# Kernel optimization log

Hardware: AMD Instinct MI355X
Metric: run time of the kernel (lower is better)

## Reference

```python
import jax, jax.numpy as jnp
import numpy as np

B, T, C, H = 2, 2048, 1024, 16
D = C // H  # head dim 64

def setup_inputs() -> dict:
    key = jax.random.key(0)
    k1, k2, k3 = jax.random.split(key, 3)
    x = jax.random.normal(k1, (B, T, C), dtype=jnp.float32)
    W_attn = jax.random.normal(k2, (C, 3 * C), dtype=jnp.float32) * (1.0 / np.sqrt(C))
    b_attn = jnp.zeros((3 * C,), dtype=jnp.float32)
    W_proj = jax.random.normal(k3, (C, C), dtype=jnp.float32) * (1.0 / np.sqrt(C))
    b_proj = jnp.zeros((C,), dtype=jnp.float32)
    return {"x": x, "W_attn": W_attn, "b_attn": b_attn, "W_proj": W_proj, "b_proj": b_proj}

def reference(x, W_attn, b_attn, W_proj, b_proj):
    Bsz, Tlen, Cdim = x.shape
    qkv = x @ W_attn + b_attn  # [B,T,3C]
    q, k, v = jnp.split(qkv, 3, axis=2)
    # [B,T,C] -> [B,H,T,D]
    q = q.reshape(Bsz, Tlen, H, D).transpose(0, 2, 1, 3)
    k = k.reshape(Bsz, Tlen, H, D).transpose(0, 2, 1, 3)
    v = v.reshape(Bsz, Tlen, H, D).transpose(0, 2, 1, 3)
    att = jnp.einsum('bhqd,bhkd->bhqk', q, k) * (1.0 / np.sqrt(D))
    causal = jnp.tril(jnp.ones((Tlen, Tlen), dtype=bool))
    att = jnp.where(causal[None, None, :, :], att, jnp.float32(-jnp.inf))
    att = jax.nn.softmax(att, axis=-1)
    y = jnp.einsum('bhqk,bhkd->bhqd', att, v)  # [B,H,T,D]
    y = y.transpose(0, 2, 1, 3).reshape(Bsz, Tlen, Cdim)
    return y @ W_proj + b_proj
```

## Files before the change

kernel.cpp:

```cpp
#include <hip/hip_runtime.h>
#include <math.h>

#define BSZ 2
#define TSEQ 2048
#define CDIM 1024
#define HNUM 16

typedef __attribute__((ext_vector_type(8))) short bhalf8;
typedef __attribute__((ext_vector_type(4))) short bhalf4;
typedef __attribute__((ext_vector_type(4))) float floatx4;

__device__ __forceinline__ unsigned short f2bf(float f) {
    union { float f; unsigned u; } v;
    v.f = f;
    unsigned r = v.u + 0x7FFFu + ((v.u >> 16) & 1u);
    return (unsigned short)(r >> 16);
}

typedef __attribute__((address_space(3))) unsigned int lds_u32;
typedef const __attribute__((address_space(1))) unsigned int g_u32;
__device__ __forceinline__ void async_copy16(const void* g, void* l) {
    __builtin_amdgcn_global_load_lds((g_u32*)g, (lds_u32*)l, 16, 0, 0);
}

#if __has_builtin(__builtin_amdgcn_mfma_f32_16x16x16bf16_1k)
#define HAVE_MFMA16 1
#define VT_PITCH 76
#else
#define HAVE_MFMA16 0
#define VT_PITCH 72
#endif

__global__ __launch_bounds__(256) void conv_bf16(
    const float* __restrict__ x, unsigned short* __restrict__ xb)
{
    size_t i = ((size_t)blockIdx.x * 256 + threadIdx.x) * 8;
    float4 a = *(const float4*)(x + i);
    float4 b = *(const float4*)(x + i + 4);
    uint4 o;
    o.x = (unsigned)f2bf(a.x) | ((unsigned)f2bf(a.y) << 16);
    o.y = (unsigned)f2bf(a.z) | ((unsigned)f2bf(a.w) << 16);
    o.z = (unsigned)f2bf(b.x) | ((unsigned)f2bf(b.y) << 16);
    o.w = (unsigned)f2bf(b.z) | ((unsigned)f2bf(b.w) << 16);
    *(uint4*)(xb + i) = o;
}

__global__ __launch_bounds__(256) void transpose_bf16(
    const float* __restrict__ W, unsigned short* __restrict__ Wt, int K, int N)
{
    __shared__ float t[32][33];
    const int n0 = blockIdx.x * 32, k0 = blockIdx.y * 32;
    const int tx = threadIdx.x & 31, ty = threadIdx.x >> 5;
#pragma unroll
    for (int i = 0; i < 4; ++i)
        t[ty + i * 8][tx] = W[(size_t)(k0 + ty + i * 8) * N + n0 + tx];
    __syncthreads();
#pragma unroll
    for (int i = 0; i < 4; ++i)
        Wt[(size_t)(n0 + ty + i * 8) * K + k0 + tx] = f2bf(t[tx][ty + i * 8]);
}

template<bool OUT_BF16>
__global__ __launch_bounds__(256) void gemm_bt(
    const unsigned short* __restrict__ A, const unsigned short* __restrict__ Bt,
    const float* __restrict__ bias, void* __restrict__ Cp,
    int M, int N, int K)
{
    __shared__ unsigned short As[128 * 32];
    __shared__ unsigned short Bs[128 * 32];

    const int tid   = threadIdx.x;
    const int bm    = blockIdx.y;
    const int bn    = blockIdx.x;
    const int wave  = tid >> 6;
    const int col16 = tid & 15;
    const int quad  = (tid & 63) >> 4;
    const int wm    = (wave >> 1) * 64;
    const int wn    = (wave & 1) * 64;

    const floatx4 vzero = {0.f, 0.f, 0.f, 0.f};
    floatx4 acc[4][4];
#pragma unroll
    for (int i = 0; i < 4; ++i)
#pragma unroll
        for (int j = 0; j < 4; ++j) acc[i][j] = vzero;

    const int gr = tid >> 2;
    const int gk = (tid & 3) * 8;
    const unsigned short* Ab = A  + (size_t)(bm * 128 + gr) * K + gk;
    const unsigned short* Bb = Bt + (size_t)(bn * 128 + gr) * K + gk;
    char* AsB = (char*)As + wave * 1024;
    char* BsB = (char*)Bs + wave * 1024;

    for (int k0 = 0; k0 < K; k0 += 32) {
        __syncthreads();
        async_copy16(Ab + k0,          AsB);
        async_copy16(Ab + 64 * K + k0, AsB + 4096);
        async_copy16(Bb + k0,          BsB);
        async_copy16(Bb + 64 * K + k0, BsB + 4096);
        __syncthreads();

        bhalf8 a[4], b[4];
#pragma unroll
        for (int i = 0; i < 4; ++i)
            a[i] = *(const bhalf8*)&As[(wm + i * 16 + col16) * 32 + quad * 8];
#pragma unroll
        for (int j = 0; j < 4; ++j)
            b[j] = *(const bhalf8*)&Bs[(wn + j * 16 + col16) * 32 + quad * 8];
#pragma unroll
        for (int i = 0; i < 4; ++i)
#pragma unroll
            for (int j = 0; j < 4; ++j)
                acc[i][j] = __builtin_amdgcn_mfma_f32_16x16x32_bf16(a[i], b[j], acc[i][j], 0, 0, 0);
    }

#pragma unroll
    for (int j = 0; j < 4; ++j) {
        int col = bn * 128 + wn + j * 16 + col16;
        float bv = bias[col];
#pragma unroll
        for (int i = 0; i < 4; ++i) {
#pragma unroll
            for (int r = 0; r < 4; ++r) {
                int row = bm * 128 + wm + i * 16 + quad * 4 + r;
                float v = acc[i][j][r] + bv;
                if (OUT_BF16)
                    ((unsigned short*)Cp)[(size_t)row * N + col] = f2bf(v);
                else
                    ((float*)Cp)[(size_t)row * N + col] = v;
            }
        }
    }
}

__global__ __launch_bounds__(256) void attn_mfma(
    const unsigned short* __restrict__ qkv, unsigned short* __restrict__ yout)
{
    __shared__ unsigned short Ks[64 * 64];
    __shared__ unsigned short Vt[64][VT_PITCH];
#if !HAVE_MFMA16
    __shared__ unsigned short Ps[4][16][72];
#endif

    const int tid   = threadIdx.x;
    const int wave  = tid >> 6;
    const int col16 = tid & 15;
    const int quad  = (tid & 63) >> 4;
    const int qb    = (int)gridDim.y - 1 - (int)blockIdx.y;
    const int bh    = blockIdx.x;
    const int b     = bh >> 4;
    const int h     = bh & 15;

    const unsigned short* base  = qkv + (size_t)b * TSEQ * 3072 + h * 64;
    const unsigned short* kbase = base + CDIM;
    const unsigned short* vbase = base + 2 * CDIM;

    bhalf8 qf[2];
    {
        const unsigned short* qrow =
            base + (size_t)(qb * 64 + wave * 16 + col16) * 3072 + quad * 8;
        qf[0] = *(const bhalf8*)qrow;
        qf[1] = *(const bhalf8*)(qrow + 32);
    }

    const int krow0 = tid >> 3;
    const int kcb   = (tid & 7) ^ ((tid >> 3) & 7);
    char* ksb = (char*)Ks + wave * 1024;

    const int vr     = tid & 63;
    const int vcolg0 = (tid >> 6) * 2;

    floatx4 oT[4];
    const floatx4 vzero = {0.f, 0.f, 0.f, 0.f};
#pragma unroll
    for (int dt = 0; dt < 4; ++dt) oT[dt] = vzero;
    float l_part = 0.f;

    const float C_MUL = 0.125f * 1.44269504f;
    const float C_SUB = 17.31234049f;
    const int   qloc  = wave * 16 + col16;

    for (int kb = 0; kb <= qb; ++kb) {
        __syncthreads();
        async_copy16(kbase + (size_t)(kb * 64 + krow0) * 3072 + kcb * 8, ksb);
        async_copy16(kbase + (size_t)(kb * 64 + 32 + krow0) * 3072 + kcb * 8, ksb + 4096);
        {
            const unsigned short* vrow = vbase + (size_t)(kb * 64 + vr) * 3072 + vcolg0 * 8;
            uint4 v0 = *(const uint4*)vrow;
            uint4 v1 = *(const uint4*)(vrow + 8);
            Vt[vcolg0 * 8 + 0][vr] = (unsigned short)(v0.x & 0xffff);
            Vt[vcolg0 * 8 + 1][vr] = (unsigned short)(v0.x >> 16);
            Vt[vcolg0 * 8 + 2][vr] = (unsigned short)(v0.y & 0xffff);
            Vt[vcolg0 * 8 + 3][vr] = (unsigned short)(v0.y >> 16);
            Vt[vcolg0 * 8 + 4][vr] = (unsigned short)(v0.z & 0xffff);
            Vt[vcolg0 * 8 + 5][vr] = (unsigned short)(v0.z >> 16);
            Vt[vcolg0 * 8 + 6][vr] = (unsigned short)(v0.w & 0xffff);
            Vt[vcolg0 * 8 + 7][vr] = (unsigned short)(v0.w >> 16);
            Vt[vcolg0 * 8 + 8][vr]  = (unsigned short)(v1.x & 0xffff);
            Vt[vcolg0 * 8 + 9][vr]  = (unsigned short)(v1.x >> 16);
            Vt[vcolg0 * 8 + 10][vr] = (unsigned short)(v1.y & 0xffff);
            Vt[vcolg0 * 8 + 11][vr] = (unsigned short)(v1.y >> 16);
            Vt[vcolg0 * 8 + 12][vr] = (unsigned short)(v1.z & 0xffff);
            Vt[vcolg0 * 8 + 13][vr] = (unsigned short)(v1.z >> 16);
            Vt[vcolg0 * 8 + 14][vr] = (unsigned short)(v1.w & 0xffff);
            Vt[vcolg0 * 8 + 15][vr] = (unsigned short)(v1.w >> 16);
        }
        __syncthreads();

        floatx4 s[4];
#pragma unroll
        for (int n = 0; n < 4; ++n) {
            const int row = 16 * n + col16;
            const int sx  = col16 & 7;
            bhalf8 k0 = *(const bhalf8*)&Ks[row * 64 + ((quad ^ sx) * 8)];
            bhalf8 k1 = *(const bhalf8*)&Ks[row * 64 + (((4 + quad) ^ sx) * 8)];
            floatx4 t = __builtin_amdgcn_mfma_f32_16x16x32_bf16(k0, qf[0], vzero, 0, 0, 0);
            s[n] = __builtin_amdgcn_mfma_f32_16x16x32_bf16(k1, qf[1], t, 0, 0, 0);
        }

#if HAVE_MFMA16
        bhalf4 pb[4];
#endif
#pragma unroll
        for (int n = 0; n < 4; ++n) {
            unsigned short u[4];
#pragma unroll
            for (int r = 0; r < 4; ++r) {
                const int kvloc = 16 * n + quad * 4 + r;
                float p;
                if (kb == qb && kvloc > qloc) p = 0.f;
                else p = exp2f(fmaf(s[n][r], C_MUL, -C_SUB));
                l_part += p;
                u[r] = f2bf(p);
            }
#if HAVE_MFMA16
            bhalf4 t = {(short)u[0], (short)u[1], (short)u[2], (short)u[3]};
            pb[n] = t;
#else
            Ps[wave][col16][16 * n + quad * 4 + 0] = u[0];
            Ps[wave][col16][16 * n + quad * 4 + 1] = u[1];
            Ps[wave][col16][16 * n + quad * 4 + 2] = u[2];
            Ps[wave][col16][16 * n + quad * 4 + 3] = u[3];
#endif
        }

#if HAVE_MFMA16
#pragma unroll
        for (int n = 0; n < 4; ++n) {
#pragma unroll
            for (int dt = 0; dt < 4; ++dt) {
                bhalf4 av = *(const bhalf4*)&Vt[16 * dt + col16][16 * n + quad * 4];
                oT[dt] = __builtin_amdgcn_mfma_f32_16x16x16bf16_1k(av, pb[n], oT[dt], 0, 0, 0);
            }
        }
#else
#pragma unroll
        for (int ks = 0; ks < 2; ++ks) {
            bhalf8 pbig = *(const bhalf8*)&Ps[wave][col16][ks * 32 + quad * 8];
#pragma unroll
            for (int dt = 0; dt < 4; ++dt) {
                bhalf8 av = *(const bhalf8*)&Vt[16 * dt + col16][ks * 32 + quad * 8];
                oT[dt] = __builtin_amdgcn_mfma_f32_16x16x32_bf16(av, pbig, oT[dt], 0, 0, 0);
            }
        }
#endif
    }

    float l = l_part;
    l += __shfl_xor(l, 16);
    l += __shfl_xor(l, 32);
    const float inv = 1.0f / l;
    const size_t row = (size_t)b * TSEQ + (size_t)qb * 64 + wave * 16 + col16;
#pragma unroll
    for (int dt = 0; dt < 4; ++dt) {
        ushort4 o;
        o.x = f2bf(oT[dt][0] * inv);
        o.y = f2bf(oT[dt][1] * inv);
        o.z = f2bf(oT[dt][2] * inv);
        o.w = f2bf(oT[dt][3] * inv);
        *(ushort4*)(yout + row * CDIM + h * 64 + 16 * dt + quad * 4) = o;
    }
}

extern "C" void kernel_launch(void* const* d_in, const int* in_sizes, int n_in,
                              void* d_out, int out_size, void* d_ws, size_t ws_size,
                              hipStream_t stream)
{
    const float* x      = (const float*)d_in[0];
    const float* W_attn = (const float*)d_in[1];
    const float* b_attn = (const float*)d_in[2];
    const float* W_proj = (const float*)d_in[3];
    const float* b_proj = (const float*)d_in[4];
    float* out = (float*)d_out;

    unsigned short* qkv = (unsigned short*)d_ws;
    unsigned short* y   = qkv + (size_t)4096 * 3072;
    unsigned short* xb  = y   + (size_t)4096 * 1024;
    unsigned short* WtA = xb  + (size_t)4096 * 1024;
    unsigned short* WtP = WtA + (size_t)3072 * 1024;

    conv_bf16<<<dim3((4096 * 1024) / (256 * 8)), 256, 0, stream>>>(x, xb);
    transpose_bf16<<<dim3(3072 / 32, 1024 / 32), 256, 0, stream>>>(W_attn, WtA, 1024, 3072);
    transpose_bf16<<<dim3(1024 / 32, 1024 / 32), 256, 0, stream>>>(W_proj, WtP, 1024, 1024);

    gemm_bt<true><<<dim3(3072 / 128, 4096 / 128), 256, 0, stream>>>(
        xb, WtA, b_attn, qkv, 4096, 3072, 1024);
    attn_mfma<<<dim3(BSZ * HNUM, TSEQ / 64), 256, 0, stream>>>(qkv, y);
    gemm_bt<false><<<dim3(1024 / 128, 4096 / 128), 256, 0, stream>>>(
        y, WtP, b_proj, out, 4096, 1024, 1024);
}
```

Before: 200.4 us.

## Write V transposed from QKV GEMM epilogue and async-load it in attention

The QKV GEMM epilogue now writes the V columns directly into a transposed [B*C, T] buffer, so the attention kernel can async-copy V tiles into swizzled LDS instead of transposing them per tile with scalar LDS stores. The attention loop is split into a template where only the diagonal tile applies the causal mask, and the bf16 packing of P uses a cheaper rounding trick. The cost is strided 2-byte global stores in the GEMM epilogue for the V region, which may hurt that GEMM's write efficiency.

New measurement: 205.7 us. 2.6% more time.

```diff
diff --git a/kernel.cpp b/kernel.cpp
--- a/kernel.cpp
+++ b/kernel.cpp
@@ -22,14 +22,6 @@
 __device__ __forceinline__ void async_copy16(const void* g, void* l) {
     __builtin_amdgcn_global_load_lds((g_u32*)g, (lds_u32*)l, 16, 0, 0);
 }
-
-#if __has_builtin(__builtin_amdgcn_mfma_f32_16x16x16bf16_1k)
-#define HAVE_MFMA16 1
-#define VT_PITCH 76
-#else
-#define HAVE_MFMA16 0
-#define VT_PITCH 72
-#endif
 
 __global__ __launch_bounds__(256) void conv_bf16(
     const float* __restrict__ x, unsigned short* __restrict__ xb)
@@ -64,7 +56,7 @@
 __global__ __launch_bounds__(256) void gemm_bt(
     const unsigned short* __restrict__ A, const unsigned short* __restrict__ Bt,
     const float* __restrict__ bias, void* __restrict__ Cp,
-    int M, int N, int K)
+    int M, int N, int K, int v_start, unsigned short* __restrict__ vt)
 {
     __shared__ unsigned short As[128 * 32];
     __shared__ unsigned short Bs[128 * 32];
@@ -114,9 +106,11 @@
                 acc[i][j] = __builtin_amdgcn_mfma_f32_16x16x32_bf16(a[i], b[j], acc[i][j], 0, 0, 0);
     }
 
+    const int colbase = bn * 128 + wn;
+    const bool vpath = (v_start >= 0) && (colbase >= v_start);
 #pragma unroll
     for (int j = 0; j < 4; ++j) {
-        int col = bn * 128 + wn + j * 16 + col16;
+        int col = colbase + j * 16 + col16;
         float bv = bias[col];
 #pragma unroll
         for (int i = 0; i < 4; ++i) {
@@ -124,23 +118,96 @@
             for (int r = 0; r < 4; ++r) {
                 int row = bm * 128 + wm + i * 16 + quad * 4 + r;
                 float v = acc[i][j][r] + bv;
-                if (OUT_BF16)
+                if (vpath) {
+                    size_t vrow = (size_t)((row >> 11) * 1024 + (col - v_start));
+                    vt[vrow * 2048 + (row & 2047)] = f2bf(v);
+                } else if (OUT_BF16) {
                     ((unsigned short*)Cp)[(size_t)row * N + col] = f2bf(v);
-                else
+                } else {
                     ((float*)Cp)[(size_t)row * N + col] = v;
+                }
             }
         }
     }
 }
 
+__device__ __forceinline__ floatx4 fx4_zero() { floatx4 z = {0.f,0.f,0.f,0.f}; return z; }
+
+template<bool DIAG>
+__device__ __forceinline__ void attn_kv_tile(
+    int kb,
+    const unsigned short* __restrict__ kbase,
+    const unsigned short* __restrict__ vtb,
+    unsigned short* Ks, unsigned short* Vt,
+    const bhalf8* qf, floatx4* oT, float& l_part,
+    int tid, int col16, int quad, int qloc)
+{
+    const float C_MUL = 0.125f * 1.44269504f;
+    const float C_SUB = 17.31234049f;
+
+    const int krow0 = tid >> 3;
+    const int kcb   = (tid & 7) ^ ((tid >> 3) & 7);
+    char* ksb = (char*)Ks + (tid >> 6) * 1024;
+    const int vc8s  = (tid & 7) ^ ((tid >> 3) & 7);
+    char* vsb = (char*)Vt + (tid >> 6) * 1024;
+
+    __syncthreads();
+    async_copy16(kbase + (size_t)(kb * 64 + krow0) * 3072 + kcb * 8, ksb);
+    async_copy16(kbase + (size_t)(kb * 64 + 32 + krow0) * 3072 + kcb * 8, ksb + 4096);
+    async_copy16(vtb + (size_t)krow0 * 2048 + kb * 64 + vc8s * 8, vsb);
+    async_copy16(vtb + (size_t)(krow0 + 32) * 2048 + kb * 64 + vc8s * 8, vsb + 4096);
+    __syncthreads();
+
+    const int sx = col16 & 7;
+    floatx4 s[4];
+#pragma unroll
+    for (int n = 0; n < 4; ++n) {
+        const int row = 16 * n + col16;
+        bhalf8 k0 = *(const bhalf8*)&Ks[row * 64 + ((quad ^ sx) * 8)];
+        bhalf8 k1 = *(const bhalf8*)&Ks[row * 64 + (((4 + quad) ^ sx) * 8)];
+        floatx4 t = __builtin_amdgcn_mfma_f32_16x16x32_bf16(k0, qf[0], fx4_zero(), 0, 0, 0);
+        s[n] = __builtin_amdgcn_mfma_f32_16x16x32_bf16(k1, qf[1], t, 0, 0, 0);
+    }
+
+    bhalf4 pb[4];
+#pragma unroll
+    for (int n = 0; n < 4; ++n) {
+        unsigned a[4];
+#pragma unroll
+        for (int r = 0; r < 4; ++r) {
+            float p = exp2f(fmaf(s[n][r], C_MUL, -C_SUB));
+            if (DIAG) {
+                const int kvloc = 16 * n + quad * 4 + r;
+                if (kvloc > qloc) p = 0.f;
+            }
+            l_part += p;
+            a[r] = __float_as_uint(p) + 0x8000u;
+        }
+        union { unsigned u[2]; bhalf4 b; } uu;
+        uu.u[0] = (a[0] >> 16) | (a[1] & 0xffff0000u);
+        uu.u[1] = (a[2] >> 16) | (a[3] & 0xffff0000u);
+        pb[n] = uu.b;
+    }
+
+#pragma unroll
+    for (int n = 0; n < 4; ++n) {
+        const int ch = 2 * n + (quad >> 1);
+#pragma unroll
+        for (int dt = 0; dt < 4; ++dt) {
+            const int d = 16 * dt + col16;
+            bhalf4 av = *(const bhalf4*)&Vt[d * 64 + ((ch ^ (d & 7)) * 8) + (quad & 1) * 4];
+            oT[dt] = __builtin_amdgcn_mfma_f32_16x16x16bf16_1k(av, pb[n], oT[dt], 0, 0, 0);
+        }
+    }
+}
+
 __global__ __launch_bounds__(256) void attn_mfma(
-    const unsigned short* __restrict__ qkv, unsigned short* __restrict__ yout)
+    const unsigned short* __restrict__ qkv,
+    const unsigned short* __restrict__ vT,
+    unsigned short* __restrict__ yout)
 {
     __shared__ unsigned short Ks[64 * 64];
-    __shared__ unsigned short Vt[64][VT_PITCH];
-#if !HAVE_MFMA16
-    __shared__ unsigned short Ps[4][16][72];
-#endif
+    __shared__ unsigned short Vt[64 * 64];
 
     const int tid   = threadIdx.x;
     const int wave  = tid >> 6;
@@ -153,7 +220,7 @@
 
     const unsigned short* base  = qkv + (size_t)b * TSEQ * 3072 + h * 64;
     const unsigned short* kbase = base + CDIM;
-    const unsigned short* vbase = base + 2 * CDIM;
+    const unsigned short* vtb   = vT + (size_t)(b * 1024 + h * 64) * 2048;
 
     bhalf8 qf[2];
     {
@@ -163,108 +230,17 @@
         qf[1] = *(const bhalf8*)(qrow + 32);
     }
 
-    const int krow0 = tid >> 3;
-    const int kcb   = (tid & 7) ^ ((tid >> 3) & 7);
-    char* ksb = (char*)Ks + wave * 1024;
-
-    const int vr     = tid & 63;
-    const int vcolg0 = (tid >> 6) * 2;
-
     floatx4 oT[4];
-    const floatx4 vzero = {0.f, 0.f, 0.f, 0.f};
-#pragma unroll
-    for (int dt = 0; dt < 4; ++dt) oT[dt] = vzero;
+#pragma unroll
+    for (int dt = 0; dt < 4; ++dt) oT[dt] = fx4_zero();
     float l_part = 0.f;
-
-    const float C_MUL = 0.125f * 1.44269504f;
-    const float C_SUB = 17.31234049f;
-    const int   qloc  = wave * 16 + col16;
-
-    for (int kb = 0; kb <= qb; ++kb) {
-        __syncthreads();
-        async_copy16(kbase + (size_t)(kb * 64 + krow0) * 3072 + kcb * 8, ksb);
-        async_copy16(kbase + (size_t)(kb * 64 + 32 + krow0) * 3072 + kcb * 8, ksb + 4096);
-        {
-            const unsigned short* vrow = vbase + (size_t)(kb * 64 + vr) * 3072 + vcolg0 * 8;
-            uint4 v0 = *(const uint4*)vrow;
-            uint4 v1 = *(const uint4*)(vrow + 8);
-            Vt[vcolg0 * 8 + 0][vr] = (unsigned short)(v0.x & 0xffff);
-            Vt[vcolg0 * 8 + 1][vr] = (unsigned short)(v0.x >> 16);
-            Vt[vcolg0 * 8 + 2][vr] = (unsigned short)(v0.y & 0xffff);
-            Vt[vcolg0 * 8 + 3][vr] = (unsigned short)(v0.y >> 16);
-            Vt[vcolg0 * 8 + 4][vr] = (unsigned short)(v0.z & 0xffff);
-            Vt[vcolg0 * 8 + 5][vr] = (unsigned short)(v0.z >> 16);
-            Vt[vcolg0 * 8 + 6][vr] = (unsigned short)(v0.w & 0xffff);
-            Vt[vcolg0 * 8 + 7][vr] = (unsigned short)(v0.w >> 16);
-            Vt[vcolg0 * 8 + 8][vr]  = (unsigned short)(v1.x & 0xffff);
-            Vt[vcolg0 * 8 + 9][vr]  = (unsigned short)(v1.x >> 16);
-            Vt[vcolg0 * 8 + 10][vr] = (unsigned short)(v1.y & 0xffff);
-            Vt[vcolg0 * 8 + 11][vr] = (unsigned short)(v1.y >> 16);
-            Vt[vcolg0 * 8 + 12][vr] = (unsigned short)(v1.z & 0xffff);
-            Vt[vcolg0 * 8 + 13][vr] = (unsigned short)(v1.z >> 16);
-            Vt[vcolg0 * 8 + 14][vr] = (unsigned short)(v1.w & 0xffff);
-            Vt[vcolg0 * 8 + 15][vr] = (unsigned short)(v1.w >> 16);
-        }
-        __syncthreads();
-
-        floatx4 s[4];
-#pragma unroll
-        for (int n = 0; n < 4; ++n) {
-            const int row = 16 * n + col16;
-            const int sx  = col16 & 7;
-            bhalf8 k0 = *(const bhalf8*)&Ks[row * 64 + ((quad ^ sx) * 8)];
-            bhalf8 k1 = *(const bhalf8*)&Ks[row * 64 + (((4 + quad) ^ sx) * 8)];
-            floatx4 t = __builtin_amdgcn_mfma_f32_16x16x32_bf16(k0, qf[0], vzero, 0, 0, 0);
-            s[n] = __builtin_amdgcn_mfma_f32_16x16x32_bf16(k1, qf[1], t, 0, 0, 0);
-        }
-
-#if HAVE_MFMA16
-        bhalf4 pb[4];
-#endif
-#pragma unroll
-        for (int n = 0; n < 4; ++n) {
-            unsigned short u[4];
-#pragma unroll
-            for (int r = 0; r < 4; ++r) {
-                const int kvloc = 16 * n + quad * 4 + r;
-                float p;
-                if (kb == qb && kvloc > qloc) p = 0.f;
-                else p = exp2f(fmaf(s[n][r], C_MUL, -C_SUB));
-                l_part += p;
-                u[r] = f2bf(p);
-            }
-#if HAVE_MFMA16
-            bhalf4 t = {(short)u[0], (short)u[1], (short)u[2], (short)u[3]};
-            pb[n] = t;
-#else
-            Ps[wave][col16][16 * n + quad * 4 + 0] = u[0];
-            Ps[wave][col16][16 * n + quad * 4 + 1] = u[1];
-            Ps[wave][col16][16 * n + quad * 4 + 2] = u[2];
-            Ps[wave][col16][16 * n + quad * 4 + 3] = u[3];
-#endif
-        }
-
-#if HAVE_MFMA16
-#pragma unroll
-        for (int n = 0; n < 4; ++n) {
-#pragma unroll
-            for (int dt = 0; dt < 4; ++dt) {
-                bhalf4 av = *(const bhalf4*)&Vt[16 * dt + col16][16 * n + quad * 4];
-                oT[dt] = __builtin_amdgcn_mfma_f32_16x16x16bf16_1k(av, pb[n], oT[dt], 0, 0, 0);
-            }
-        }
-#else
-#pragma unroll
-        for (int ks = 0; ks < 2; ++ks) {
-            bhalf8 pbig = *(const bhalf8*)&Ps[wave][col16][ks * 32 + quad * 8];
-#pragma unroll
-            for (int dt = 0; dt < 4; ++dt) {
-                bhalf8 av = *(const bhalf8*)&Vt[16 * dt + col16][ks * 32 + quad * 8];
-                oT[dt] = __builtin_amdgcn_mfma_f32_16x16x32_bf16(av, pbig, oT[dt], 0, 0, 0);
-            }
-        }
-#endif
-    }
+    const int qloc = wave * 16 + col16;
+
+    for (int kb = 0; kb < qb; ++kb)
+        attn_kv_tile<false>(kb, kbase, vtb, Ks, Vt, qf, oT, l_part,
+                            tid, col16, quad, qloc);
+    attn_kv_tile<true>(qb, kbase, vtb, Ks, Vt, qf, oT, l_part,
+                       tid, col16, quad, qloc);
 
     float l = l_part;
     l += __shfl_xor(l, 16);
@@ -298,14 +274,15 @@
     unsigned short* xb  = y   + (size_t)4096 * 1024;
     unsigned short* WtA = xb  + (size_t)4096 * 1024;
     unsigned short* WtP = WtA + (size_t)3072 * 1024;
+    unsigned short* vT  = WtP + (size_t)1024 * 1024;
 
     conv_bf16<<<dim3((4096 * 1024) / (256 * 8)), 256, 0, stream>>>(x, xb);
     transpose_bf16<<<dim3(3072 / 32, 1024 / 32), 256, 0, stream>>>(W_attn, WtA, 1024, 3072);
     transpose_bf16<<<dim3(1024 / 32, 1024 / 32), 256, 0, stream>>>(W_proj, WtP, 1024, 1024);
 
     gemm_bt<true><<<dim3(3072 / 128, 4096 / 128), 256, 0, stream>>>(
-        xb, WtA, b_attn, qkv, 4096, 3072, 1024);
-    attn_mfma<<<dim3(BSZ * HNUM, TSEQ / 64), 256, 0, stream>>>(qkv, y);
+        xb, WtA, b_attn, qkv, 4096, 3072, 1024, 2048, vT);
+    attn_mfma<<<dim3(BSZ * HNUM, TSEQ / 64), 256, 0, stream>>>(qkv, vT, y);
     gemm_bt<false><<<dim3(1024 / 128, 4096 / 128), 256, 0, stream>>>(
-        y, WtP, b_proj, out, 4096, 1024, 1024);
-}
+        y, WtP, b_proj, out, 4096, 1024, 1024, -1, nullptr);
+}
```
